# Kernel tuning notes

Measured on AMD Instinct MI355X. Metric: run time of the kernel, lower is better.

Reference implementation:

```python
import jax, jax.numpy as jnp
import numpy as np

B, S, H, NH = 4, 1024, 2048, 16
HD = H // NH  # 128


def _rotate_half(x):
    x1, x2 = jnp.split(x, 2, axis=-1)
    return jnp.concatenate([-x2, x1], axis=-1)


def setup_inputs() -> dict:
    key = jax.random.key(0)
    ks = jax.random.split(key, 8)
    hidden_states = jax.random.normal(ks[0], (B, S, H), dtype=jnp.float32)
    k_in = jax.random.normal(ks[1], (B * NH, HD, S), dtype=jnp.float32)  # [B*nh, hd, K]
    v_in = jax.random.normal(ks[2], (B, NH, S, HD), dtype=jnp.float32)   # [B, nh, K, hd]
    # causal additive mask [B, 1, Q, K]
    i = jnp.arange(S)[:, None]
    j = jnp.arange(S)[None, :]
    mask = jnp.where(j <= i, 0.0, -1e9).astype(jnp.float32)
    attention_mask = jnp.broadcast_to(mask, (B, 1, S, S))
    # RoPE tables [S, hd]
    inv_freq = 1.0 / (10000.0 ** (jnp.arange(0, HD, 2, dtype=jnp.float32) / HD))
    freqs = jnp.arange(S, dtype=jnp.float32)[:, None] * inv_freq[None, :]  # [S, hd/2]
    emb = jnp.concatenate([freqs, freqs], axis=-1)  # [S, hd]
    rope_cos = jnp.cos(emb)
    rope_sin = jnp.sin(emb)
    std = 0.02
    wq = jax.random.normal(ks[3], (H, H), dtype=jnp.float32) * std
    bq = jnp.zeros((H,), dtype=jnp.float32)
    wo = jax.random.normal(ks[4], (H, H), dtype=jnp.float32) * (std / np.sqrt(2 * 24))
    bo = jnp.zeros((H,), dtype=jnp.float32)
    return {"hidden_states": hidden_states, "key": k_in, "value": v_in,
            "attention_mask": attention_mask, "rope_cos": rope_cos,
            "rope_sin": rope_sin, "wq": wq, "bq": bq, "wo": wo, "bo": bo}


def reference(hidden_states, key, value, attention_mask, rope_cos, rope_sin, wq, bq, wo, bo):
    dtype = hidden_states.dtype
    scale = 1.0 / np.sqrt(HD)
    # q projection -> [B, nh, Q, hd]
    q = hidden_states @ wq.T + bq
    q = q.reshape(B, S, NH, HD).transpose(0, 2, 1, 3)
    # RoPE on query only
    cos = rope_cos[None, None, :, :]
    sin = rope_sin[None, None, :, :]
    q = q * cos + _rotate_half(q) * sin
    # scores: key is [B*nh, hd, K]
    k = key.reshape(B, NH, HD, S)
    scores = jnp.einsum('bhqd,bhdk->bhqk', q, k) * scale + attention_mask
    probs = jax.nn.softmax(scores.astype(jnp.float32), axis=-1).astype(dtype)
    # attention output -> [B, Q, H]
    out = jnp.einsum('bhqk,bhkd->bqhd', probs, value).reshape(B, S, H)
    out = out @ wo.T + bo
    return out
```

## Files before the change

kernel.cpp:

```cpp
#include <hip/hip_runtime.h>
#include <cstdint>


typedef unsigned short u16;
typedef __bf16 bf16x8 __attribute__((ext_vector_type(8)));
typedef float  f32x4  __attribute__((ext_vector_type(4)));
typedef float  f32x16 __attribute__((ext_vector_type(16)));
typedef uint32_t u32x4 __attribute__((ext_vector_type(4)));

__device__ __forceinline__ u16 f2bf(float f) {
  uint32_t u = __builtin_bit_cast(uint32_t, f);
  u += 0x7fffu + ((u >> 16) & 1u);
  return (u16)(u >> 16);
}
__device__ __forceinline__ uint32_t cvtpk(float lo, float hi) {
  uint32_t r;
  asm("v_cvt_pk_bf16_f32 %0, %1, %2" : "=v"(r) : "v"(lo), "v"(hi));
  return r;
}
__device__ __forceinline__ void gld16(const void* g, void* l) {
  __builtin_amdgcn_global_load_lds(
      (const __attribute__((address_space(1))) void*)g,
      (__attribute__((address_space(3))) void*)l, 16, 0, 0);
}

__global__ __launch_bounds__(256) void cvt_all(const float* __restrict__ hs,
                                               const float* __restrict__ wq,
                                               const float* __restrict__ wo,
                                               u16* __restrict__ hs_o,
                                               u16* __restrict__ wq_o,
                                               u16* __restrict__ wo_o) {
  int i = blockIdx.x * 256 + threadIdx.x;
  const float* in;
  u16* out;
  int j;
  if (i < 2097152)      { in = hs; out = hs_o; j = i; }
  else if (i < 3145728) { in = wq; out = wq_o; j = i - 2097152; }
  else                  { in = wo; out = wo_o; j = i - 3145728; }
  float4 v = ((const float4*)in)[j];
  ushort4 o;
  o.x = f2bf(v.x); o.y = f2bf(v.y); o.z = f2bf(v.z); o.w = f2bf(v.w);
  ((ushort4*)out)[j] = o;
}

__global__ __launch_bounds__(256) void transpose_cvt(const float* __restrict__ in,
                                                     u16* __restrict__ out, int R, int C) {
  __shared__ float tile[32][33];
  const int bh = blockIdx.x;
  const int nct = C >> 5;
  const int rt = blockIdx.y / nct, ct = blockIdx.y % nct;
  const float* src = in + (size_t)bh * R * C;
  u16* dst = out + (size_t)bh * R * C;
  const int r = threadIdx.x >> 3, c4 = (threadIdx.x & 7) * 4;
  float4 v = *(const float4*)(src + (size_t)(rt * 32 + r) * C + ct * 32 + c4);
  tile[r][c4 + 0] = v.x; tile[r][c4 + 1] = v.y;
  tile[r][c4 + 2] = v.z; tile[r][c4 + 3] = v.w;
  __syncthreads();
  ushort4 o;
  o.x = f2bf(tile[c4 + 0][r]); o.y = f2bf(tile[c4 + 1][r]);
  o.z = f2bf(tile[c4 + 2][r]); o.w = f2bf(tile[c4 + 3][r]);
  *(ushort4*)(dst + (size_t)(ct * 32 + r) * R + rt * 32 + c4) = o;
}

template<int MODE>
__global__ __launch_bounds__(512, 1)
void gemm256(const u16* __restrict__ A, const u16* __restrict__ Bm,
             const float* __restrict__ bias, const float* __restrict__ cosb,
             const float* __restrict__ sinb, void* __restrict__ Cout) {
  constexpr int K = 2048, N = 2048, NT = 32;
  __shared__ __align__(16) u16 LA[3][256 * 64];
  __shared__ __align__(16) u16 LB[3][128 * 64];
  const int t = threadIdx.x, lane = t & 63, w = t >> 6;
  const int row0 = blockIdx.x * 256, col0 = blockIdx.y * 128;
  const int wr = (w >> 1) * 64;
  const int g = w & 1;
  const int fr = lane & 15, fg = lane >> 4, fx = fr & 7;
  const int sb8 = ((t & 7) ^ ((t >> 3) & 7)) * 8;
  const u16* gA = A  + (size_t)(row0 + (t >> 3)) * K + sb8;
  const u16* gB = Bm + (size_t)(col0 + (t >> 3)) * K + sb8;
  const int lo8 = t * 8;

  int brow[4];
  if constexpr (MODE == 1) {
    brow[0] = g * 32 + fr;      brow[1] = g * 32 + 16 + fr;
    brow[2] = g * 32 + 64 + fr; brow[3] = g * 32 + 80 + fr;
  } else {
    brow[0] = g * 64 + fr;      brow[1] = g * 64 + 16 + fr;
    brow[2] = g * 64 + 32 + fr; brow[3] = g * 64 + 48 + fr;
  }

  f32x4 acc[4][4] = {};

  auto SA0 = [&](int kt, int buf) {
    const int k0 = kt * 64;
    gld16(gA + k0,                    &LA[buf][lo8]);
    gld16(gA + k0 + (size_t)64 * K,   &LA[buf][4096 + lo8]);
    gld16(gB + k0,                    &LB[buf][lo8]);
  };
  auto SA1 = [&](int kt, int buf) {
    const int k0 = kt * 64;
    gld16(gA + k0 + (size_t)128 * K,  &LA[buf][8192 + lo8]);
    gld16(gA + k0 + (size_t)192 * K,  &LA[buf][12288 + lo8]);
    gld16(gB + k0 + (size_t)64 * K,   &LB[buf][4096 + lo8]);
  };

  SA0(0, 0); SA1(0, 0);
  SA0(1, 1); SA1(1, 1);

  int cb = 0;
  for (int kt = 0; kt < NT; ++kt) {
    const int sbuf = cb >= 1 ? cb - 1 : cb + 2;
    if (kt < NT - 1) asm volatile("s_waitcnt vmcnt(6)" ::: "memory");
    else             asm volatile("s_waitcnt vmcnt(0)" ::: "memory");
    __builtin_amdgcn_s_barrier();
    asm volatile("" ::: "memory");

    bf16x8 af[4][2], bq0[2][2];
#pragma unroll
    for (int mi = 0; mi < 4; mi++)
#pragma unroll
      for (int ks = 0; ks < 2; ks++)
        af[mi][ks] = *(const bf16x8*)&LA[cb][(wr + mi * 16 + fr) * 64 + ((ks * 4 + fg) ^ fx) * 8];
#pragma unroll
    for (int ni = 0; ni < 2; ni++)
#pragma unroll
      for (int ks = 0; ks < 2; ks++)
        bq0[ni][ks] = *(const bf16x8*)&LB[cb][brow[ni] * 64 + ((ks * 4 + fg) ^ fx) * 8];
    if (kt + 2 < NT) SA0(kt + 2, sbuf);
    __builtin_amdgcn_s_setprio(1);
#pragma unroll
    for (int ks = 0; ks < 2; ks++)
#pragma unroll
      for (int mi = 0; mi < 4; mi++)
#pragma unroll
        for (int ni = 0; ni < 2; ni++)
          acc[mi][ni] = __builtin_amdgcn_mfma_f32_16x16x32_bf16(af[mi][ks], bq0[ni][ks], acc[mi][ni], 0, 0, 0);
    __builtin_amdgcn_s_setprio(0);
    __builtin_amdgcn_s_barrier();
    asm volatile("" ::: "memory");

    bf16x8 bq1[2][2];
#pragma unroll
    for (int ni = 0; ni < 2; ni++)
#pragma unroll
      for (int ks = 0; ks < 2; ks++)
        bq1[ni][ks] = *(const bf16x8*)&LB[cb][brow[ni + 2] * 64 + ((ks * 4 + fg) ^ fx) * 8];
    if (kt + 2 < NT) SA1(kt + 2, sbuf);
    __builtin_amdgcn_s_setprio(1);
#pragma unroll
    for (int ks = 0; ks < 2; ks++)
#pragma unroll
      for (int mi = 0; mi < 4; mi++)
#pragma unroll
        for (int ni = 0; ni < 2; ni++)
          acc[mi][ni + 2] = __builtin_amdgcn_mfma_f32_16x16x32_bf16(af[mi][ks], bq1[ni][ks], acc[mi][ni + 2], 0, 0, 0);
    __builtin_amdgcn_s_setprio(0);

    cb = cb == 2 ? 0 : cb + 1;
  }

  if constexpr (MODE == 0) {
#pragma unroll
    for (int mi = 0; mi < 4; mi++)
#pragma unroll
      for (int ni = 0; ni < 4; ni++) {
        int col = col0 + brow[ni];
        float bv = bias[col];
#pragma unroll
        for (int i = 0; i < 4; i++) {
          int row = row0 + wr + mi * 16 + fg * 4 + i;
          ((float*)Cout)[(size_t)row * N + col] = acc[mi][ni][i] + bv;
        }
      }
  } else {
    const int h = blockIdx.y;
    const float SL2E = 0.12751743f;
    float bv[4];
#pragma unroll
    for (int ni = 0; ni < 4; ni++) bv[ni] = bias[h * 128 + brow[ni]];
    u16* qout = (u16*)Cout;
#pragma unroll
    for (int mi = 0; mi < 4; mi++)
#pragma unroll
      for (int i = 0; i < 4; i++) {
        int row = row0 + wr + mi * 16 + fg * 4 + i;
        int s = row & 1023, bb = row >> 10;
        size_t obase = (((size_t)(bb * 16 + h)) * 1024 + s) * 128;
#pragma unroll
        for (int dp = 0; dp < 2; dp++) {
          int d = g * 32 + dp * 16 + fr;
          float c  = cosb[s * 128 + d] * SL2E;
          float sn = sinb[s * 128 + d] * SL2E;
          float qlo = acc[mi][dp][i] + bv[dp];
          float qhi = acc[mi][dp + 2][i] + bv[dp + 2];
          qout[obase + d]      = f2bf(qlo * c - qhi * sn);
          qout[obase + d + 64] = f2bf(qhi * c + qlo * sn);
        }
      }
  }
}

__global__ __launch_bounds__(256, 1)
void attn_kernel(const u16* __restrict__ qbf, const u16* __restrict__ kTb,
                 const u16* __restrict__ vTb, u16* __restrict__ aout) {
  __shared__ __align__(16) u16 Kb[2][64 * 128];
  __shared__ __align__(16) u16 Vb[2][128 * 64];
  const int t = threadIdx.x, lane = t & 63, w = t >> 6;
  const int x = blockIdx.x;
  const int qt = 7 - (x >> 6);
  const int bh = x & 63;
  const int b = bh >> 4, h = bh & 15;
  const int q31 = lane & 31, hi = lane >> 5, kx7 = q31 & 7;
  const u16* kbase = kTb + (size_t)bh * 131072;
  const u16* vbase = vTb + (size_t)bh * 131072;

  const int kRow = t >> 4;
  const int kCb  = (t & 15) ^ (kRow & 7);
  const int vRow = t >> 3;
  const int vCb  = (t & 7) ^ (vRow & 7);

  const int rw0 = qt * 128 + w * 32;
  const int rowg = rw0 + q31;
  const int last = 2 * qt + 1;
  const int wlast = 2 * qt + (w >> 1);

  bf16x8 qf[8];
#pragma unroll
  for (int ds = 0; ds < 8; ds++)
    qf[ds] = *(const bf16x8*)&qbf[((size_t)bh * 1024 + rowg) * 128 + ds * 16 + hi * 8];

  f32x16 acc[4] = {};
  float m = -3e38f, l = 0.f;

  auto STAGE = [&](int kt, int buf) {
    const u16* ks = kbase + (size_t)(kt * 64 + kRow) * 128 + kCb * 8;
    const u16* vs = vbase + (size_t)vRow * 1024 + kt * 64 + vCb * 8;
    u16* kl = &Kb[buf][t * 8];
    u16* vl = &Vb[buf][t * 8];
#pragma unroll
    for (int p = 0; p < 4; p++) {
      gld16(ks + (size_t)p * 16 * 128, kl + p * 2048);
      gld16(vs + (size_t)p * 32 * 1024, vl + p * 2048);
    }
  };

  STAGE(0, 0);
  __syncthreads();
  for (int kt = 0; kt <= last; kt++) {
    const int cur = kt & 1;
    if (kt < last) STAGE(kt + 1, cur ^ 1);
    if (kt <= wlast) {
      f32x16 sa0 = {}, sa1 = {};
      __builtin_amdgcn_s_setprio(1);
#pragma unroll
      for (int ds = 0; ds < 8; ds++) {
        bf16x8 k0 = *(const bf16x8*)&Kb[cur][q31 * 128 + (((2 * ds + hi) ^ kx7) * 8)];
        bf16x8 k1 = *(const bf16x8*)&Kb[cur][(q31 + 32) * 128 + (((2 * ds + hi) ^ kx7) * 8)];
        sa0 = __builtin_amdgcn_mfma_f32_32x32x16_bf16(k0, qf[ds], sa0, 0, 0, 0);
        sa1 = __builtin_amdgcn_mfma_f32_32x32x16_bf16(k1, qf[ds], sa1, 0, 0, 0);
      }
      __builtin_amdgcn_s_setprio(0);

      if (kt == wlast) {
#pragma unroll
        for (int rr = 0; rr < 16; rr++) {
          int cr = (rr & 3) + 8 * (rr >> 2) + 4 * hi;
          if (kt * 64 + cr > rowg)      sa0[rr] = -1e9f;
          if (kt * 64 + 32 + cr > rowg) sa1[rr] = -1e9f;
        }
      }
      float t0 = fmaxf(fmaxf(sa0[0], sa0[1]), sa0[2]);
      float t1 = fmaxf(fmaxf(sa0[3], sa0[4]), sa0[5]);
      float t2 = fmaxf(fmaxf(sa0[6], sa0[7]), sa0[8]);
      float t3 = fmaxf(fmaxf(sa0[9], sa0[10]), sa0[11]);
      float t4 = fmaxf(fmaxf(sa0[12], sa0[13]), sa0[14]);
      float u0 = fmaxf(fmaxf(sa1[0], sa1[1]), sa1[2]);
      float u1 = fmaxf(fmaxf(sa1[3], sa1[4]), sa1[5]);
      float u2 = fmaxf(fmaxf(sa1[6], sa1[7]), sa1[8]);
      float u3 = fmaxf(fmaxf(sa1[9], sa1[10]), sa1[11]);
      float u4 = fmaxf(fmaxf(sa1[12], sa1[13]), sa1[14]);
      float mx = fmaxf(fmaxf(fmaxf(fmaxf(t0, t1), fmaxf(t2, t3)),
                             fmaxf(fmaxf(t4, sa0[15]), fmaxf(u0, u1))),
                       fmaxf(fmaxf(u2, u3), fmaxf(u4, sa1[15])));
      mx = fmaxf(mx, __shfl_xor(mx, 32));
      if (!__all(mx - m <= 11.5f)) {
        float mn = fmaxf(m, mx);
        float corr = __builtin_amdgcn_exp2f(m - mn);
        m = mn; l *= corr;
#pragma unroll
        for (int nd = 0; nd < 4; nd++)
#pragma unroll
          for (int rr = 0; rr < 16; rr++) acc[nd][rr] *= corr;
      }
#pragma unroll
      for (int rr = 0; rr < 16; rr++) {
        sa0[rr] = __builtin_amdgcn_exp2f(sa0[rr] - m);
        sa1[rr] = __builtin_amdgcn_exp2f(sa1[rr] - m);
      }
      {
        float s0 = (sa0[0] + sa0[1]) + (sa0[2] + sa0[3]);
        float s1 = (sa0[4] + sa0[5]) + (sa0[6] + sa0[7]);
        float s2 = (sa0[8] + sa0[9]) + (sa0[10] + sa0[11]);
        float s3 = (sa0[12] + sa0[13]) + (sa0[14] + sa0[15]);
        float s4 = (sa1[0] + sa1[1]) + (sa1[2] + sa1[3]);
        float s5 = (sa1[4] + sa1[5]) + (sa1[6] + sa1[7]);
        float s6 = (sa1[8] + sa1[9]) + (sa1[10] + sa1[11]);
        float s7 = (sa1[12] + sa1[13]) + (sa1[14] + sa1[15]);
        float sum = ((s0 + s1) + (s2 + s3)) + ((s4 + s5) + (s6 + s7));
        sum += __shfl_xor(sum, 32);
        l += sum;
      }

      __builtin_amdgcn_s_setprio(1);
      uint32_t wA = cvtpk(sa0[0], sa0[1]),   wB = cvtpk(sa0[2], sa0[3]);
      uint32_t wC = cvtpk(sa0[4], sa0[5]),   wD = cvtpk(sa0[6], sa0[7]);
      uint32_t wE = cvtpk(sa0[8], sa0[9]),   wF = cvtpk(sa0[10], sa0[11]);
      uint32_t wG = cvtpk(sa0[12], sa0[13]), wH = cvtpk(sa0[14], sa0[15]);
      uint32_t wI = cvtpk(sa1[0], sa1[1]),   wJ = cvtpk(sa1[2], sa1[3]);
      uint32_t wK = cvtpk(sa1[4], sa1[5]),   wL = cvtpk(sa1[6], sa1[7]);
      uint32_t wM = cvtpk(sa1[8], sa1[9]),   wN = cvtpk(sa1[10], sa1[11]);
      uint32_t wO = cvtpk(sa1[12], sa1[13]), wP = cvtpk(sa1[14], sa1[15]);
      uint32_t xA = __shfl_xor(wA, 32), xB = __shfl_xor(wB, 32);
      uint32_t xC = __shfl_xor(wC, 32), xD = __shfl_xor(wD, 32);
      uint32_t xE = __shfl_xor(wE, 32), xF = __shfl_xor(wF, 32);
      uint32_t xG = __shfl_xor(wG, 32), xH = __shfl_xor(wH, 32);
      uint32_t xI = __shfl_xor(wI, 32), xJ = __shfl_xor(wJ, 32);
      uint32_t xK = __shfl_xor(wK, 32), xL = __shfl_xor(wL, 32);
      uint32_t xM = __shfl_xor(wM, 32), xN = __shfl_xor(wN, 32);
      uint32_t xO = __shfl_xor(wO, 32), xP = __shfl_xor(wP, 32);
#pragma unroll
      for (int ks = 0; ks < 4; ks++) {
        u32x4 aw;
        if (ks == 0) {
          aw.x = hi ? xC : wA;  aw.y = hi ? xD : wB;
          aw.z = hi ? wC : xA;  aw.w = hi ? wD : xB;
        } else if (ks == 1) {
          aw.x = hi ? xG : wE;  aw.y = hi ? xH : wF;
          aw.z = hi ? wG : xE;  aw.w = hi ? wH : xF;
        } else if (ks == 2) {
          aw.x = hi ? xK : wI;  aw.y = hi ? xL : wJ;
          aw.z = hi ? wK : xI;  aw.w = hi ? wL : xJ;
        } else {
          aw.x = hi ? xO : wM;  aw.y = hi ? xP : wN;
          aw.z = hi ? wO : xM;  aw.w = hi ? wP : xN;
        }
        bf16x8 af = __builtin_bit_cast(bf16x8, aw);
#pragma unroll
        for (int nd = 0; nd < 4; nd++) {
          bf16x8 vf = *(const bf16x8*)&Vb[cur][(nd * 32 + q31) * 64 + (((2 * ks + hi) ^ kx7) * 8)];
          acc[nd] = __builtin_amdgcn_mfma_f32_32x32x16_bf16(af, vf, acc[nd], 0, 0, 0);
        }
      }
      __builtin_amdgcn_s_setprio(0);
    }
    __syncthreads();
  }

  float linv = 1.f / l;
#pragma unroll
  for (int rr = 0; rr < 16; rr++) {
    int cr = (rr & 3) + 8 * (rr >> 2) + 4 * hi;
    float li = __shfl(linv, cr);
    int sg = rw0 + cr;
    size_t obase = (((size_t)b * 1024 + sg) * 16 + h) * 128 + q31;
#pragma unroll
    for (int nd = 0; nd < 4; nd++)
      aout[obase + nd * 32] = f2bf(acc[nd][rr] * li);
  }
}

extern "C" void kernel_launch(void* const* d_in, const int* in_sizes, int n_in,
                              void* d_out, int out_size, void* d_ws, size_t ws_size,
                              hipStream_t stream) {
  const float* hs  = (const float*)d_in[0];
  const float* key = (const float*)d_in[1];
  const float* val = (const float*)d_in[2];
  const float* rc  = (const float*)d_in[4];
  const float* rs  = (const float*)d_in[5];
  const float* wq  = (const float*)d_in[6];
  const float* bq  = (const float*)d_in[7];
  const float* wo  = (const float*)d_in[8];
  const float* bo  = (const float*)d_in[9];
  float* out = (float*)d_out;

  char* ws = (char*)d_ws;
  u16* hs_bf = (u16*)(ws);
  u16* wq_bf = (u16*)(ws + 16777216);
  u16* wo_bf = (u16*)(ws + 25165824);
  u16* q_bf  = (u16*)(ws + 33554432);
  u16* kT    = (u16*)(ws + 50331648);
  u16* vT    = (u16*)(ws + 67108864);
  u16* attn_bf = hs_bf;

  cvt_all<<<16384, 256, 0, stream>>>(hs, wq, wo, hs_bf, wq_bf, wo_bf);

  transpose_cvt<<<dim3(64, 128), 256, 0, stream>>>(key, kT, 128, 1024);
  transpose_cvt<<<dim3(64, 128), 256, 0, stream>>>(val, vT, 1024, 128);

  gemm256<1><<<dim3(16, 16), 512, 0, stream>>>(hs_bf, wq_bf, bq, rc, rs, q_bf);
  attn_kernel<<<512, 256, 0, stream>>>(q_bf, kT, vT, attn_bf);
  gemm256<0><<<dim3(16, 16), 512, 0, stream>>>(attn_bf, wo_bf, bo, nullptr, nullptr, out);
}
```

Baseline: 154.0 us.

## Merge prep kernels and shrink attention KV tile for higher occupancy

The three preprocessing launches (bf16 conversion plus the K and V transposes) become a single prep kernel that branches on block index, which removes launch gaps. The attention kernel's KV tile drops from 64 to 32 keys, halving shared memory and score registers, and launch bounds allow 3 blocks per CU so more waves can hide latency. The cost is twice as many loop iterations, with more barriers and more online-softmax rescale and reduction steps per key processed.

Measured after the change: 149.3 us. -3.1%, faster.

```diff
diff --git a/kernel.cpp b/kernel.cpp
--- a/kernel.cpp
+++ b/kernel.cpp
@@ -24,34 +24,36 @@
       (__attribute__((address_space(3))) void*)l, 16, 0, 0);
 }
 
-__global__ __launch_bounds__(256) void cvt_all(const float* __restrict__ hs,
-                                               const float* __restrict__ wq,
-                                               const float* __restrict__ wo,
-                                               u16* __restrict__ hs_o,
-                                               u16* __restrict__ wq_o,
-                                               u16* __restrict__ wo_o) {
-  int i = blockIdx.x * 256 + threadIdx.x;
-  const float* in;
-  u16* out;
-  int j;
-  if (i < 2097152)      { in = hs; out = hs_o; j = i; }
-  else if (i < 3145728) { in = wq; out = wq_o; j = i - 2097152; }
-  else                  { in = wo; out = wo_o; j = i - 3145728; }
-  float4 v = ((const float4*)in)[j];
-  ushort4 o;
-  o.x = f2bf(v.x); o.y = f2bf(v.y); o.z = f2bf(v.z); o.w = f2bf(v.w);
-  ((ushort4*)out)[j] = o;
-}
-
-__global__ __launch_bounds__(256) void transpose_cvt(const float* __restrict__ in,
-                                                     u16* __restrict__ out, int R, int C) {
+__global__ __launch_bounds__(256)
+void prep_kernel(const float* __restrict__ hs, const float* __restrict__ wq,
+                 const float* __restrict__ wo, const float* __restrict__ key,
+                 const float* __restrict__ val,
+                 u16* __restrict__ hs_o, u16* __restrict__ wq_o,
+                 u16* __restrict__ wo_o, u16* __restrict__ kT,
+                 u16* __restrict__ vT) {
   __shared__ float tile[32][33];
-  const int bh = blockIdx.x;
+  const int bx = blockIdx.x, tid = threadIdx.x;
+  if (bx < 16384) {
+    int i = bx * 256 + tid;
+    const float* in; u16* out; int j;
+    if (i < 2097152)      { in = hs; out = hs_o; j = i; }
+    else if (i < 3145728) { in = wq; out = wq_o; j = i - 2097152; }
+    else                  { in = wo; out = wo_o; j = i - 3145728; }
+    float4 v = ((const float4*)in)[j];
+    ushort4 o;
+    o.x = f2bf(v.x); o.y = f2bf(v.y); o.z = f2bf(v.z); o.w = f2bf(v.w);
+    ((ushort4*)out)[j] = o;
+    return;
+  }
+  const bool isK = bx < 24576;
+  const int idx = bx - (isK ? 16384 : 24576);
+  const int R = isK ? 128 : 1024, C = isK ? 1024 : 128;
+  const int bh = idx >> 7, y = idx & 127;
   const int nct = C >> 5;
-  const int rt = blockIdx.y / nct, ct = blockIdx.y % nct;
-  const float* src = in + (size_t)bh * R * C;
-  u16* dst = out + (size_t)bh * R * C;
-  const int r = threadIdx.x >> 3, c4 = (threadIdx.x & 7) * 4;
+  const int rt = y / nct, ct = y % nct;
+  const float* src = (isK ? key : val) + (size_t)bh * 131072;
+  u16* dst = (isK ? kT : vT) + (size_t)bh * 131072;
+  const int r = tid >> 3, c4 = (tid & 7) * 4;
   float4 v = *(const float4*)(src + (size_t)(rt * 32 + r) * C + ct * 32 + c4);
   tile[r][c4 + 0] = v.x; tile[r][c4 + 1] = v.y;
   tile[r][c4 + 2] = v.z; tile[r][c4 + 3] = v.w;
@@ -200,29 +202,30 @@
   }
 }
 
-__global__ __launch_bounds__(256, 1)
+__global__ __launch_bounds__(256, 3)
 void attn_kernel(const u16* __restrict__ qbf, const u16* __restrict__ kTb,
                  const u16* __restrict__ vTb, u16* __restrict__ aout) {
-  __shared__ __align__(16) u16 Kb[2][64 * 128];
-  __shared__ __align__(16) u16 Vb[2][128 * 64];
+  __shared__ __align__(16) u16 Kb[2][32 * 128];
+  __shared__ __align__(16) u16 Vb[2][128 * 32];
   const int t = threadIdx.x, lane = t & 63, w = t >> 6;
   const int x = blockIdx.x;
   const int qt = 7 - (x >> 6);
   const int bh = x & 63;
   const int b = bh >> 4, h = bh & 15;
-  const int q31 = lane & 31, hi = lane >> 5, kx7 = q31 & 7;
+  const int q31 = lane & 31, hi = lane >> 5;
+  const int kx7 = q31 & 7, kx3 = q31 & 3;
   const u16* kbase = kTb + (size_t)bh * 131072;
   const u16* vbase = vTb + (size_t)bh * 131072;
 
   const int kRow = t >> 4;
   const int kCb  = (t & 15) ^ (kRow & 7);
-  const int vRow = t >> 3;
-  const int vCb  = (t & 7) ^ (vRow & 7);
+  const int vRow = t >> 2;
+  const int vCb  = (t & 3) ^ (vRow & 3);
 
   const int rw0 = qt * 128 + w * 32;
   const int rowg = rw0 + q31;
-  const int last = 2 * qt + 1;
-  const int wlast = 2 * qt + (w >> 1);
+  const int last = qt * 4 + 3;
+  const int wlast = qt * 4 + w;
 
   bf16x8 qf[8];
 #pragma unroll
@@ -233,14 +236,14 @@
   float m = -3e38f, l = 0.f;
 
   auto STAGE = [&](int kt, int buf) {
-    const u16* ks = kbase + (size_t)(kt * 64 + kRow) * 128 + kCb * 8;
-    const u16* vs = vbase + (size_t)vRow * 1024 + kt * 64 + vCb * 8;
+    const u16* ks = kbase + (size_t)(kt * 32 + kRow) * 128 + kCb * 8;
+    const u16* vs = vbase + (size_t)vRow * 1024 + kt * 32 + vCb * 8;
     u16* kl = &Kb[buf][t * 8];
     u16* vl = &Vb[buf][t * 8];
 #pragma unroll
-    for (int p = 0; p < 4; p++) {
+    for (int p = 0; p < 2; p++) {
       gld16(ks + (size_t)p * 16 * 128, kl + p * 2048);
-      gld16(vs + (size_t)p * 32 * 1024, vl + p * 2048);
+      gld16(vs + (size_t)p * 64 * 1024, vl + p * 2048);
     }
   };
 
@@ -250,14 +253,12 @@
     const int cur = kt & 1;
     if (kt < last) STAGE(kt + 1, cur ^ 1);
     if (kt <= wlast) {
-      f32x16 sa0 = {}, sa1 = {};
+      f32x16 sa = {};
       __builtin_amdgcn_s_setprio(1);
 #pragma unroll
       for (int ds = 0; ds < 8; ds++) {
-        bf16x8 k0 = *(const bf16x8*)&Kb[cur][q31 * 128 + (((2 * ds + hi) ^ kx7) * 8)];
-        bf16x8 k1 = *(const bf16x8*)&Kb[cur][(q31 + 32) * 128 + (((2 * ds + hi) ^ kx7) * 8)];
-        sa0 = __builtin_amdgcn_mfma_f32_32x32x16_bf16(k0, qf[ds], sa0, 0, 0, 0);
-        sa1 = __builtin_amdgcn_mfma_f32_32x32x16_bf16(k1, qf[ds], sa1, 0, 0, 0);
+        bf16x8 kf = *(const bf16x8*)&Kb[cur][q31 * 128 + (((2 * ds + hi) ^ kx7) * 8)];
+        sa = __builtin_amdgcn_mfma_f32_32x32x16_bf16(kf, qf[ds], sa, 0, 0, 0);
       }
       __builtin_amdgcn_s_setprio(0);
 
@@ -265,23 +266,16 @@
 #pragma unroll
         for (int rr = 0; rr < 16; rr++) {
           int cr = (rr & 3) + 8 * (rr >> 2) + 4 * hi;
-          if (kt * 64 + cr > rowg)      sa0[rr] = -1e9f;
-          if (kt * 64 + 32 + cr > rowg) sa1[rr] = -1e9f;
-        }
-      }
-      float t0 = fmaxf(fmaxf(sa0[0], sa0[1]), sa0[2]);
-      float t1 = fmaxf(fmaxf(sa0[3], sa0[4]), sa0[5]);
-      float t2 = fmaxf(fmaxf(sa0[6], sa0[7]), sa0[8]);
-      float t3 = fmaxf(fmaxf(sa0[9], sa0[10]), sa0[11]);
-      float t4 = fmaxf(fmaxf(sa0[12], sa0[13]), sa0[14]);
-      float u0 = fmaxf(fmaxf(sa1[0], sa1[1]), sa1[2]);
-      float u1 = fmaxf(fmaxf(sa1[3], sa1[4]), sa1[5]);
-      float u2 = fmaxf(fmaxf(sa1[6], sa1[7]), sa1[8]);
-      float u3 = fmaxf(fmaxf(sa1[9], sa1[10]), sa1[11]);
-      float u4 = fmaxf(fmaxf(sa1[12], sa1[13]), sa1[14]);
-      float mx = fmaxf(fmaxf(fmaxf(fmaxf(t0, t1), fmaxf(t2, t3)),
-                             fmaxf(fmaxf(t4, sa0[15]), fmaxf(u0, u1))),
-                       fmaxf(fmaxf(u2, u3), fmaxf(u4, sa1[15])));
+          if (kt * 32 + cr > rowg) sa[rr] = -1e9f;
+        }
+      }
+      float t0 = fmaxf(fmaxf(sa[0], sa[1]), sa[2]);
+      float t1 = fmaxf(fmaxf(sa[3], sa[4]), sa[5]);
+      float t2 = fmaxf(fmaxf(sa[6], sa[7]), sa[8]);
+      float t3 = fmaxf(fmaxf(sa[9], sa[10]), sa[11]);
+      float t4 = fmaxf(fmaxf(sa[12], sa[13]), sa[14]);
+      float mx = fmaxf(fmaxf(fmaxf(t0, t1), t2),
+                       fmaxf(fmaxf(t3, t4), sa[15]));
       mx = fmaxf(mx, __shfl_xor(mx, 32));
       if (!__all(mx - m <= 11.5f)) {
         float mn = fmaxf(m, mx);
@@ -293,61 +287,40 @@
           for (int rr = 0; rr < 16; rr++) acc[nd][rr] *= corr;
       }
 #pragma unroll
-      for (int rr = 0; rr < 16; rr++) {
-        sa0[rr] = __builtin_amdgcn_exp2f(sa0[rr] - m);
-        sa1[rr] = __builtin_amdgcn_exp2f(sa1[rr] - m);
-      }
+      for (int rr = 0; rr < 16; rr++) sa[rr] = __builtin_amdgcn_exp2f(sa[rr] - m);
       {
-        float s0 = (sa0[0] + sa0[1]) + (sa0[2] + sa0[3]);
-        float s1 = (sa0[4] + sa0[5]) + (sa0[6] + sa0[7]);
-        float s2 = (sa0[8] + sa0[9]) + (sa0[10] + sa0[11]);
-        float s3 = (sa0[12] + sa0[13]) + (sa0[14] + sa0[15]);
-        float s4 = (sa1[0] + sa1[1]) + (sa1[2] + sa1[3]);
-        float s5 = (sa1[4] + sa1[5]) + (sa1[6] + sa1[7]);
-        float s6 = (sa1[8] + sa1[9]) + (sa1[10] + sa1[11]);
-        float s7 = (sa1[12] + sa1[13]) + (sa1[14] + sa1[15]);
-        float sum = ((s0 + s1) + (s2 + s3)) + ((s4 + s5) + (s6 + s7));
+        float s0 = (sa[0] + sa[1]) + (sa[2] + sa[3]);
+        float s1 = (sa[4] + sa[5]) + (sa[6] + sa[7]);
+        float s2 = (sa[8] + sa[9]) + (sa[10] + sa[11]);
+        float s3 = (sa[12] + sa[13]) + (sa[14] + sa[15]);
+        float sum = (s0 + s1) + (s2 + s3);
         sum += __shfl_xor(sum, 32);
         l += sum;
       }
 
       __builtin_amdgcn_s_setprio(1);
-      uint32_t wA = cvtpk(sa0[0], sa0[1]),   wB = cvtpk(sa0[2], sa0[3]);
-      uint32_t wC = cvtpk(sa0[4], sa0[5]),   wD = cvtpk(sa0[6], sa0[7]);
-      uint32_t wE = cvtpk(sa0[8], sa0[9]),   wF = cvtpk(sa0[10], sa0[11]);
-      uint32_t wG = cvtpk(sa0[12], sa0[13]), wH = cvtpk(sa0[14], sa0[15]);
-      uint32_t wI = cvtpk(sa1[0], sa1[1]),   wJ = cvtpk(sa1[2], sa1[3]);
-      uint32_t wK = cvtpk(sa1[4], sa1[5]),   wL = cvtpk(sa1[6], sa1[7]);
-      uint32_t wM = cvtpk(sa1[8], sa1[9]),   wN = cvtpk(sa1[10], sa1[11]);
-      uint32_t wO = cvtpk(sa1[12], sa1[13]), wP = cvtpk(sa1[14], sa1[15]);
+      uint32_t wA = cvtpk(sa[0], sa[1]),   wB = cvtpk(sa[2], sa[3]);
+      uint32_t wC = cvtpk(sa[4], sa[5]),   wD = cvtpk(sa[6], sa[7]);
+      uint32_t wE = cvtpk(sa[8], sa[9]),   wF = cvtpk(sa[10], sa[11]);
+      uint32_t wG = cvtpk(sa[12], sa[13]), wH = cvtpk(sa[14], sa[15]);
       uint32_t xA = __shfl_xor(wA, 32), xB = __shfl_xor(wB, 32);
       uint32_t xC = __shfl_xor(wC, 32), xD = __shfl_xor(wD, 32);
       uint32_t xE = __shfl_xor(wE, 32), xF = __shfl_xor(wF, 32);
       uint32_t xG = __shfl_xor(wG, 32), xH = __shfl_xor(wH, 32);
-      uint32_t xI = __shfl_xor(wI, 32), xJ = __shfl_xor(wJ, 32);
-      uint32_t xK = __shfl_xor(wK, 32), xL = __shfl_xor(wL, 32);
-      uint32_t xM = __shfl_xor(wM, 32), xN = __shfl_xor(wN, 32);
-      uint32_t xO = __shfl_xor(wO, 32), xP = __shfl_xor(wP, 32);
-#pragma unroll
-      for (int ks = 0; ks < 4; ks++) {
+#pragma unroll
+      for (int ks = 0; ks < 2; ks++) {
         u32x4 aw;
         if (ks == 0) {
           aw.x = hi ? xC : wA;  aw.y = hi ? xD : wB;
           aw.z = hi ? wC : xA;  aw.w = hi ? wD : xB;
-        } else if (ks == 1) {
+        } else {
           aw.x = hi ? xG : wE;  aw.y = hi ? xH : wF;
           aw.z = hi ? wG : xE;  aw.w = hi ? wH : xF;
-        } else if (ks == 2) {
-          aw.x = hi ? xK : wI;  aw.y = hi ? xL : wJ;
-          aw.z = hi ? wK : xI;  aw.w = hi ? wL : xJ;
-        } else {
-          aw.x = hi ? xO : wM;  aw.y = hi ? xP : wN;
-          aw.z = hi ? wO : xM;  aw.w = hi ? wP : xN;
         }
         bf16x8 af = __builtin_bit_cast(bf16x8, aw);
 #pragma unroll
         for (int nd = 0; nd < 4; nd++) {
-          bf16x8 vf = *(const bf16x8*)&Vb[cur][(nd * 32 + q31) * 64 + (((2 * ks + hi) ^ kx7) * 8)];
+          bf16x8 vf = *(const bf16x8*)&Vb[cur][(nd * 32 + q31) * 32 + (((2 * ks + hi) ^ kx3) * 8)];
           acc[nd] = __builtin_amdgcn_mfma_f32_32x32x16_bf16(af, vf, acc[nd], 0, 0, 0);
         }
       }
@@ -392,10 +365,8 @@
   u16* vT    = (u16*)(ws + 67108864);
   u16* attn_bf = hs_bf;
 
-  cvt_all<<<16384, 256, 0, stream>>>(hs, wq, wo, hs_bf, wq_bf, wo_bf);
-
-  transpose_cvt<<<dim3(64, 128), 256, 0, stream>>>(key, kT, 128, 1024);
-  transpose_cvt<<<dim3(64, 128), 256, 0, stream>>>(val, vT, 1024, 128);
+  prep_kernel<<<32768, 256, 0, stream>>>(hs, wq, wo, key, val,
+                                         hs_bf, wq_bf, wo_bf, kT, vT);
 
   gemm256<1><<<dim3(16, 16), 512, 0, stream>>>(hs_bf, wq_bf, bq, rc, rs, q_bf);
   attn_kernel<<<512, 256, 0, stream>>>(q_bf, kT, vT, attn_bf);
```
